# Performance work log

Hardware: AMD Instinct MI355X
Metric: run time of the kernel (lower is better)

## Reference

```python
import jax, jax.numpy as jnp
import numpy as np

B, D, K = 32, 64, 26      # batch, n_objects, per-object feature dim
QST = 256                  # question embedding size
G = [512, 512, 512, 512, 512, 512, 28]  # g_layers (last = n_answers)
IN = 2 * K                 # in_size = concat(x_i, x_j)
AGG = 4                    # aggregation + question injection position


def setup_inputs() -> dict:
    key = jax.random.key(0)
    ks = jax.random.split(key, 2 + 2 * len(G))
    inp = {
        "x": jax.random.normal(ks[0], (B, D, K), jnp.float32),
        "qst": jax.random.normal(ks[1], (B, QST), jnp.float32),
    }
    prev = IN
    for i, g in enumerate(G):
        d_in = prev + (QST if i == AGG else 0)
        inp[f"W{i}"] = jax.random.normal(ks[2 + 2 * i], (g, d_in), jnp.float32) * (1.0 / np.sqrt(d_in))
        inp[f"b{i}"] = jnp.zeros((g,), jnp.float32)
        prev = g
    return inp


def reference(x, qst, W0, b0, W1, b1, W2, b2, W3, b3, W4, b4, W5, b5, W6, b6):
    b, d, k = x.shape
    # all ordered pairs: x_full[b, p, q] = [x[b, q], x[b, p]]  (matches torch repeat/cat order)
    xi = jnp.broadcast_to(x[:, None, :, :], (b, d, d, k))
    xj = jnp.broadcast_to(x[:, :, None, :], (b, d, d, k))
    h = jnp.concatenate([xi, xj], axis=-1).reshape(b * d * d, 2 * k)
    Ws = [W0, W1, W2, W3, W4, W5, W6]
    bs = [b0, b1, b2, b3, b4, b5, b6]
    n = len(Ws)
    for i in range(n):
        if i == AGG:
            # sum-aggregation over all d^2 pairs, then question injection
            h = h.reshape(b, d * d, h.shape[-1]).sum(axis=1)  # [b, g]
            h = jnp.concatenate([h, qst], axis=1)             # [b, g+qst]
        h = h @ Ws[i].T + bs[i]
        if i != n - 1:
            h = jax.nn.relu(h)
    return jax.nn.log_softmax(h, axis=1)
```

## Files before the change

kernel.cpp:

```cpp
#include <hip/hip_runtime.h>
#include <math.h>


typedef __attribute__((ext_vector_type(8))) short bf16x8;
typedef __attribute__((ext_vector_type(4))) float f32x4;
typedef __attribute__((ext_vector_type(4))) unsigned int u32x4;

__device__ __forceinline__ unsigned short f2bf(float f) {
    union { float f; unsigned u; } x; x.f = f;
    unsigned r = x.u + 0x7fffu + ((x.u >> 16) & 1u);
    return (unsigned short)(r >> 16);
}

#define NPV_WP   98304
#define NPV_W0P  4096
#define NPV_W4   98304
#define NPV_W5   65536
#define NPV_TOTAL (NPV_WP + NPV_W0P + NPV_W4 + NPV_W5)
__global__ void k_prep(const float* __restrict__ W1, const float* __restrict__ W2,
                       const float* __restrict__ W3, const float* __restrict__ W0,
                       const float* __restrict__ W4, const float* __restrict__ W5,
                       unsigned short* __restrict__ Wp,
                       unsigned short* __restrict__ W0p,
                       float* __restrict__ W4v,
                       float* __restrict__ W5v)
{
    int f = blockIdx.x * 256 + threadIdx.x;
    if (f < NPV_WP) {
        int l = f >> 15, r = f & 32767;
        int n = r >> 6, kq = r & 63;
        const float* W = (l == 0) ? W1 : (l == 1) ? W2 : W3;
        const float* src = W + n * 512 + kq * 8;
        int s = kq >> 2, q4 = kq & 3;
        int wv = n >> 6, jj = (n >> 4) & 3, i16 = n & 15;
        int lane = q4 * 16 + i16;
        unsigned w[4];
        #pragma unroll
        for (int h = 0; h < 4; ++h)
            w[h] = (unsigned)f2bf(src[h * 2]) | ((unsigned)f2bf(src[h * 2 + 1]) << 16);
        *(u32x4*)(Wp + (size_t)l * 262144 + ((((wv * 16 + s) * 4 + jj) * 64 + lane) << 3))
            = (u32x4){w[0], w[1], w[2], w[3]};
    } else if (f < NPV_WP + NPV_W0P) {
        int g = f - NPV_WP;
        int n = g >> 3, kq = g & 7;
        int s = kq >> 2, q4 = kq & 3;
        int wv = n >> 6, jj = (n >> 4) & 3, i16 = n & 15;
        int lane = q4 * 16 + i16;
        unsigned w[4];
        #pragma unroll
        for (int h = 0; h < 4; ++h) {
            int k0 = kq * 8 + h * 2, k1 = k0 + 1;
            float f0 = (k0 < 52) ? W0[n * 52 + k0] : 0.f;
            float f1 = (k1 < 52) ? W0[n * 52 + k1] : 0.f;
            w[h] = (unsigned)f2bf(f0) | ((unsigned)f2bf(f1) << 16);
        }
        *(u32x4*)(W0p + ((((wv * 2 + s) * 4 + jj) * 64 + lane) << 3))
            = (u32x4){w[0], w[1], w[2], w[3]};
    } else if (f < NPV_WP + NPV_W0P + NPV_W4) {
        int g = f - (NPV_WP + NPV_W0P);
        int o = g / 192, kb = g % 192;
        float4 w = *(const float4*)(W4 + (size_t)o * 768 + kb * 4);
        *(float4*)(W4v + (size_t)kb * 2048 + o * 4) = w;
    } else {
        int g = f - (NPV_WP + NPV_W0P + NPV_W4);
        int o = g >> 7, kb = g & 127;
        float4 w = *(const float4*)(W5 + (size_t)o * 512 + kb * 4);
        *(float4*)(W5v + (size_t)kb * 2048 + o * 4) = w;
    }
}

__device__ __forceinline__ void store_h(const f32x4 (&acc)[4][4], const float* __restrict__ bl,
                                        unsigned short* hbuf, int wave, int i16, int q4, int lane)
{
    char* base = (char*)hbuf;
    #pragma unroll
    for (int j = 0; j < 4; ++j) {
        int col = (wave * 4 + j) * 16 + i16;
        int g = col >> 3;
        int e = g & 7;
        float bb = bl[col];
        char* colbase = base + g * 1024 + ((col & 7) << 1);
        #pragma unroll
        for (int mt = 0; mt < 4; ++mt) {
            #pragma unroll
            for (int r = 0; r < 4; ++r) {
                int row = mt * 16 + q4 * 4 + r;
                float v = fmaxf(acc[mt][j][r] + bb, 0.f);
                int vi = __float_as_int(v);
                int swi = __builtin_amdgcn_update_dpp(0, vi, 0xB1, 0xF, 0xF, true);
                if ((lane & 1) == 0) {
                    unsigned pk;
                    asm("v_cvt_pk_bf16_f32 %0, %1, %2" : "=v"(pk) : "v"(vi), "v"(swi));
                    int slot = row ^ e;
                    *(unsigned*)(colbase + slot * 16) = pk;
                }
            }
        }
    }
}

#define CLUSTER(AV0, AV1, AV2, AV3, BV, JJ)                                              \
    __builtin_amdgcn_s_setprio(1);                                                      \
    acc[0][JJ] = __builtin_amdgcn_mfma_f32_16x16x32_bf16(AV0, BV, acc[0][JJ], 0, 0, 0); \
    acc[1][JJ] = __builtin_amdgcn_mfma_f32_16x16x32_bf16(AV1, BV, acc[1][JJ], 0, 0, 0); \
    acc[2][JJ] = __builtin_amdgcn_mfma_f32_16x16x32_bf16(AV2, BV, acc[2][JJ], 0, 0, 0); \
    acc[3][JJ] = __builtin_amdgcn_mfma_f32_16x16x32_bf16(AV3, BV, acc[3][JJ], 0, 0, 0); \
    __builtin_amdgcn_s_setprio(0);                                                      \
    __builtin_amdgcn_sched_barrier(0);

__global__ __launch_bounds__(512, 2) void k_fused(
    const float* __restrict__ x,
    const unsigned short* __restrict__ Wp,
    const unsigned short* __restrict__ W0p,
    const float* __restrict__ b0, const float* __restrict__ b1,
    const float* __restrict__ b2, const float* __restrict__ b3,
    float* __restrict__ P)
{
    __shared__ __align__(16) unsigned short hsm[2 * 64 * 512];
    __shared__ __align__(16) unsigned short xs[8 * 64 * 8];
    int t = threadIdx.x;
    int blk = blockIdx.x;
    int b = blk >> 6, p = blk & 63;

    {
        int row = t >> 3, gr = t & 7;
        const float* xq = x + (size_t)(b * 64 + row) * 26;
        const float* xp = x + (size_t)(b * 64 + p) * 26;
        unsigned w[4];
        #pragma unroll
        for (int h = 0; h < 4; ++h) {
            int k0 = gr * 8 + h * 2;
            int k1 = k0 + 1;
            float f0 = (k0 < 26) ? xq[k0] : (k0 < 52 ? xp[k0 - 26] : 0.f);
            float f1 = (k1 < 26) ? xq[k1] : (k1 < 52 ? xp[k1 - 26] : 0.f);
            w[h] = (unsigned)f2bf(f0) | ((unsigned)f2bf(f1) << 16);
        }
        *(u32x4*)((char*)xs + gr * 1024 + ((row ^ gr) << 4)) = (u32x4){w[0], w[1], w[2], w[3]};
    }

    int wave = t >> 6, lane = t & 63;
    int i16 = lane & 15, q4 = lane >> 4;

    f32x4 acc[4][4];
    bf16x8 X0, X1, X2, X3, Y0, Y1, Y2, Y3;

    const unsigned short* Bb0base = Wp + wave * 32768 + lane * 8;

    __syncthreads();

    {
        #pragma unroll
        for (int mt = 0; mt < 4; ++mt)
            #pragma unroll
            for (int j = 0; j < 4; ++j)
                acc[mt][j] = (f32x4){0.f, 0.f, 0.f, 0.f};
        const unsigned short* Bw0 = W0p + wave * 4096 + lane * 8;
        const char* xb = (const char*)xs;
        #pragma unroll
        for (int s = 0; s < 2; ++s) {
            bf16x8 bfr[4];
            #pragma unroll
            for (int j = 0; j < 4; ++j)
                bfr[j] = *(const bf16x8*)(Bw0 + s * 2048 + j * 512);
            int g = s * 4 + q4;
            const char* A0 = xb + g * 1024 + ((i16 ^ g) << 4);
            #pragma unroll
            for (int mt = 0; mt < 4; ++mt) {
                bf16x8 a = *(const bf16x8*)(A0 + mt * 256);
                #pragma unroll
                for (int j = 0; j < 4; ++j)
                    acc[mt][j] = __builtin_amdgcn_mfma_f32_16x16x32_bf16(a, bfr[j], acc[mt][j], 0, 0, 0);
            }
        }
        X0 = *(const bf16x8*)(Bb0base);
        X1 = *(const bf16x8*)(Bb0base + 512);
        X2 = *(const bf16x8*)(Bb0base + 1024);
        X3 = *(const bf16x8*)(Bb0base + 1536);
        Y0 = *(const bf16x8*)(Bb0base + 2048);
        Y1 = *(const bf16x8*)(Bb0base + 2560);
        Y2 = *(const bf16x8*)(Bb0base + 3072);
        Y3 = *(const bf16x8*)(Bb0base + 3584);
        store_h(acc, b0, hsm, wave, i16, q4, lane);
    }
    __syncthreads();

    int A_even = (q4 << 10) + ((i16 ^ q4) << 4);
    int A_odd  = 4096 + (A_even ^ 64);

    #pragma unroll 1
    for (int l = 0; l < 3; ++l) {
        const float* bl = (l == 0) ? b1 : (l == 1) ? b2 : b3;
        const unsigned short* Bb = Bb0base + (size_t)l * 262144;
        const char* hb = (const char*)hsm + (l & 1) * 65536;
        const char* hbe = hb + A_even;
        const char* hbo = hb + A_odd;

        #pragma unroll
        for (int mt = 0; mt < 4; ++mt)
            #pragma unroll
            for (int j = 0; j < 4; ++j)
                acc[mt][j] = (f32x4){0.f, 0.f, 0.f, 0.f};

        bf16x8 aE0 = *(const bf16x8*)(hbe);
        bf16x8 aE1 = *(const bf16x8*)(hbe + 256);
        bf16x8 aE2 = *(const bf16x8*)(hbe + 512);
        bf16x8 aE3 = *(const bf16x8*)(hbe + 768);
        bf16x8 aO0, aO1, aO2, aO3;

        #pragma unroll 1
        for (int s = 0; s < 16; s += 2) {
            {
                const unsigned short* BX = Bb + ((s + 2 < 16) ? (s + 2) : 14) * 2048;
                const char* po = hbo + (s << 12);
                CLUSTER(aE0, aE1, aE2, aE3, X0, 0)
                X0 = *(const bf16x8*)(BX);
                aO0 = *(const bf16x8*)(po);
                aO1 = *(const bf16x8*)(po + 256);
                CLUSTER(aE0, aE1, aE2, aE3, X1, 1)
                X1 = *(const bf16x8*)(BX + 512);
                aO2 = *(const bf16x8*)(po + 512);
                aO3 = *(const bf16x8*)(po + 768);
                CLUSTER(aE0, aE1, aE2, aE3, X2, 2)
                X2 = *(const bf16x8*)(BX + 1024);
                CLUSTER(aE0, aE1, aE2, aE3, X3, 3)
                X3 = *(const bf16x8*)(BX + 1536);
            }
            {
                const unsigned short* BY = Bb + ((s + 3 < 16) ? (s + 3) : 15) * 2048;
                const char* pe = hbe + ((s + 2 < 16 ? s + 2 : 14) << 12);
                CLUSTER(aO0, aO1, aO2, aO3, Y0, 0)
                Y0 = *(const bf16x8*)(BY);
                aE0 = *(const bf16x8*)(pe);
                aE1 = *(const bf16x8*)(pe + 256);
                CLUSTER(aO0, aO1, aO2, aO3, Y1, 1)
                Y1 = *(const bf16x8*)(BY + 512);
                aE2 = *(const bf16x8*)(pe + 512);
                aE3 = *(const bf16x8*)(pe + 768);
                CLUSTER(aO0, aO1, aO2, aO3, Y2, 2)
                Y2 = *(const bf16x8*)(BY + 1024);
                CLUSTER(aO0, aO1, aO2, aO3, Y3, 3)
                Y3 = *(const bf16x8*)(BY + 1536);
            }
        }

        if (l < 2) {
            const unsigned short* Bn = Bb + 262144;
            X0 = *(const bf16x8*)(Bn);
            X1 = *(const bf16x8*)(Bn + 512);
            X2 = *(const bf16x8*)(Bn + 1024);
            X3 = *(const bf16x8*)(Bn + 1536);
            Y0 = *(const bf16x8*)(Bn + 2048);
            Y1 = *(const bf16x8*)(Bn + 2560);
            Y2 = *(const bf16x8*)(Bn + 3072);
            Y3 = *(const bf16x8*)(Bn + 3584);
            store_h(acc, bl, (unsigned short*)((char*)hsm + ((l + 1) & 1) * 65536),
                    wave, i16, q4, lane);
            __syncthreads();
        } else {
            #pragma unroll
            for (int j = 0; j < 4; ++j) {
                int col = (wave * 4 + j) * 16 + i16;
                float bb = bl[col];
                float sum = 0.f;
                #pragma unroll
                for (int mt = 0; mt < 4; ++mt)
                    #pragma unroll
                    for (int r = 0; r < 4; ++r)
                        sum += fmaxf(acc[mt][j][r] + bb, 0.f);
                sum += __shfl_xor(sum, 16);
                sum += __shfl_xor(sum, 32);
                if (q4 == 0) P[(size_t)blk * 512 + col] = sum;
            }
        }
    }
}

__global__ __launch_bounds__(64) void k_t1(const float* __restrict__ P,
                                           float* __restrict__ Z)
{
    int b = blockIdx.x >> 3, sl = blockIdx.x & 7;
    int col = sl * 64 + threadIdx.x;
    const float* Pb = P + (size_t)b * 64 * 512 + col;
    float s = 0.f;
    #pragma unroll 8
    for (int c = 0; c < 64; ++c) s += Pb[c * 512];
    Z[b * 512 + col] = s;
}

__global__ __launch_bounds__(256) void k_t2(
    const float* __restrict__ Z, const float* __restrict__ qst,
    const float* __restrict__ W4v, const float* __restrict__ b4,
    float* __restrict__ H4)
{
    int b = blockIdx.x >> 3, sl = blockIdx.x & 7;
    int t = threadIdx.x;
    __shared__ __align__(16) float z[768];
    __shared__ float ps[256];
    for (int i = t; i < 768; i += 256)
        z[i] = (i < 512) ? Z[b * 512 + i] : qst[b * 256 + (i - 512)];
    __syncthreads();
    int o = sl * 64 + (t & 63), hf = t >> 6;
    float acc = 0.f;
    const float4* Wv = (const float4*)W4v;
    const float4* z4 = (const float4*)z;
    #pragma unroll 4
    for (int kb = hf * 48; kb < hf * 48 + 48; ++kb) {
        float4 w = Wv[kb * 512 + o];
        float4 zz = z4[kb];
        acc = fmaf(w.x, zz.x, acc);
        acc = fmaf(w.y, zz.y, acc);
        acc = fmaf(w.z, zz.z, acc);
        acc = fmaf(w.w, zz.w, acc);
    }
    ps[t] = acc;
    __syncthreads();
    if (t < 64)
        H4[b * 512 + o] = fmaxf(ps[t] + ps[t + 64] + ps[t + 128] + ps[t + 192] + b4[o], 0.f);
}

__global__ __launch_bounds__(256) void k_t3(
    const float* __restrict__ H4,
    const float* __restrict__ W5v, const float* __restrict__ b5,
    float* __restrict__ H5)
{
    int b = blockIdx.x >> 3, sl = blockIdx.x & 7;
    int t = threadIdx.x;
    __shared__ __align__(16) float h4[512];
    __shared__ float ps[256];
    for (int i = t; i < 512; i += 256) h4[i] = H4[b * 512 + i];
    __syncthreads();
    int o = sl * 64 + (t & 63), hf = t >> 6;
    float acc = 0.f;
    const float4* Wv = (const float4*)W5v;
    const float4* h44 = (const float4*)h4;
    #pragma unroll 4
    for (int kb = hf * 32; kb < hf * 32 + 32; ++kb) {
        float4 w = Wv[kb * 512 + o];
        float4 hh = h44[kb];
        acc = fmaf(w.x, hh.x, acc);
        acc = fmaf(w.y, hh.y, acc);
        acc = fmaf(w.z, hh.z, acc);
        acc = fmaf(w.w, hh.w, acc);
    }
    ps[t] = acc;
    __syncthreads();
    if (t < 64)
        H5[b * 512 + o] = fmaxf(ps[t] + ps[t + 64] + ps[t + 128] + ps[t + 192] + b5[o], 0.f);
}

__global__ __launch_bounds__(512) void k_t4(
    const float* __restrict__ H5,
    const float* __restrict__ W6, const float* __restrict__ b6,
    float* __restrict__ out)
{
    int b = blockIdx.x, t = threadIdx.x;
    __shared__ __align__(16) float h5[512];
    __shared__ float logits[28];
    __shared__ float red[2];
    h5[t] = H5[b * 512 + t];
    __syncthreads();
    {
        int o = t >> 4, c = t & 15;
        if (o < 28) {
            float acc = 0.f;
            for (int k = c; k < 512; k += 16) acc = fmaf(W6[o * 512 + k], h5[k], acc);
            acc += __shfl_xor(acc, 1);
            acc += __shfl_xor(acc, 2);
            acc += __shfl_xor(acc, 4);
            acc += __shfl_xor(acc, 8);
            if (c == 0) logits[o] = acc + b6[o];
        }
    }
    __syncthreads();
    if (t == 0) {
        float mx = -1e30f;
        for (int cc = 0; cc < 28; ++cc) mx = fmaxf(mx, logits[cc]);
        float se = 0.f;
        for (int cc = 0; cc < 28; ++cc) se += expf(logits[cc] - mx);
        red[0] = mx; red[1] = logf(se);
    }
    __syncthreads();
    if (t < 28) out[b * 28 + t] = logits[t] - red[0] - red[1];
}

extern "C" void kernel_launch(void* const* d_in, const int* in_sizes, int n_in,
                              void* d_out, int out_size, void* d_ws, size_t ws_size,
                              hipStream_t stream)
{
    const float* x   = (const float*)d_in[0];
    const float* qst = (const float*)d_in[1];
    const float* W0  = (const float*)d_in[2];
    const float* b0  = (const float*)d_in[3];
    const float* W1  = (const float*)d_in[4];
    const float* b1  = (const float*)d_in[5];
    const float* W2  = (const float*)d_in[6];
    const float* b2  = (const float*)d_in[7];
    const float* W3  = (const float*)d_in[8];
    const float* b3  = (const float*)d_in[9];
    const float* W4  = (const float*)d_in[10];
    const float* b4  = (const float*)d_in[11];
    const float* W5  = (const float*)d_in[12];
    const float* b5  = (const float*)d_in[13];
    const float* W6  = (const float*)d_in[14];
    const float* b6  = (const float*)d_in[15];
    float* out = (float*)d_out;

    char* ws = (char*)d_ws;
    unsigned short* Wp  = (unsigned short*)(ws);
    unsigned short* W0p = (unsigned short*)(ws + 1572864);
    float*          W4v = (float*)(ws + 1638400);
    float*          W5v = (float*)(ws + 3211264);
    float*          P   = (float*)(ws + 4259840);
    float*          Z   = (float*)(ws + 8454144);
    float*          H4  = (float*)(ws + 8519680);
    float*          H5  = (float*)(ws + 8585216);

    k_prep <<<NPV_TOTAL / 256, 256, 0, stream>>>(W1, W2, W3, W0, W4, W5,
                                                 Wp, W0p, W4v, W5v);
    k_fused<<<2048, 512, 0, stream>>>(x, Wp, W0p, b0, b1, b2, b3, P);
    k_t1   <<<256, 64, 0, stream>>>(P, Z);
    k_t2   <<<256, 256, 0, stream>>>(Z, qst, W4v, b4, H4);
    k_t3   <<<256, 256, 0, stream>>>(H4, W5v, b5, H5);
    k_t4   <<<32, 512, 0, stream>>>(H5, W6, b6, out);
}
```

Baseline: 314.2 us.

## Stream weight tiles via global_load_lds double buffer and single-buffer activations

Replaces register-held weight B-fragment prefetch with direct global-to-LDS async loads (global_load_lds) into a per-wave double-buffered staging area, synchronized with vmcnt waits. To fit LDS, the ping-pong activation buffer is collapsed into a single buffer, adding an extra __syncthreads before each layer's store. The intent is to free VGPRs and hide weight-load latency. The cost is extra LDS reads per step, an added barrier per layer, and a manual vmcnt(4) wait whose correctness depends on the exact instruction ordering.

```diff
diff --git a/kernel.cpp b/kernel.cpp
--- a/kernel.cpp
+++ b/kernel.cpp
@@ -11,6 +11,15 @@
     unsigned r = x.u + 0x7fffu + ((x.u >> 16) & 1u);
     return (unsigned short)(r >> 16);
 }
+
+#define GLDS16(G, L)                                                        \
+    __builtin_amdgcn_global_load_lds(                                       \
+        (const __attribute__((address_space(1))) void*)(G),                 \
+        (__attribute__((address_space(3))) void*)(L), 16, 0, 0)
+
+#define WAIT_SLOT()                                        \
+    asm volatile("s_waitcnt vmcnt(4)" ::: "memory");       \
+    __builtin_amdgcn_sched_barrier(0);
 
 #define NPV_WP   98304
 #define NPV_W0P  4096
@@ -116,7 +125,8 @@
     const float* __restrict__ b2, const float* __restrict__ b3,
     float* __restrict__ P)
 {
-    __shared__ __align__(16) unsigned short hsm[2 * 64 * 512];
+    __shared__ __align__(16) unsigned short hsm[64 * 512];
+    __shared__ __align__(16) unsigned short Bst[2 * 8 * 2048];
     __shared__ __align__(16) unsigned short xs[8 * 64 * 8];
     int t = threadIdx.x;
     int blk = blockIdx.x;
@@ -142,9 +152,11 @@
     int i16 = lane & 15, q4 = lane >> 4;
 
     f32x4 acc[4][4];
-    bf16x8 X0, X1, X2, X3, Y0, Y1, Y2, Y3;
 
     const unsigned short* Bb0base = Wp + wave * 32768 + lane * 8;
+    unsigned short* Bw0 = Bst + wave * 2048;
+    unsigned short* Bw1 = Bw0 + 16384;
+    const char* Brd = (const char*)Bst + wave * 4096 + lane * 16;
 
     __syncthreads();
 
@@ -154,14 +166,14 @@
             #pragma unroll
             for (int j = 0; j < 4; ++j)
                 acc[mt][j] = (f32x4){0.f, 0.f, 0.f, 0.f};
-        const unsigned short* Bw0 = W0p + wave * 4096 + lane * 8;
+        const unsigned short* Bw = W0p + wave * 4096 + lane * 8;
         const char* xb = (const char*)xs;
         #pragma unroll
         for (int s = 0; s < 2; ++s) {
             bf16x8 bfr[4];
             #pragma unroll
             for (int j = 0; j < 4; ++j)
-                bfr[j] = *(const bf16x8*)(Bw0 + s * 2048 + j * 512);
+                bfr[j] = *(const bf16x8*)(Bw + s * 2048 + j * 512);
             int g = s * 4 + q4;
             const char* A0 = xb + g * 1024 + ((i16 ^ g) << 4);
             #pragma unroll
@@ -172,28 +184,22 @@
                     acc[mt][j] = __builtin_amdgcn_mfma_f32_16x16x32_bf16(a, bfr[j], acc[mt][j], 0, 0, 0);
             }
         }
-        X0 = *(const bf16x8*)(Bb0base);
-        X1 = *(const bf16x8*)(Bb0base + 512);
-        X2 = *(const bf16x8*)(Bb0base + 1024);
-        X3 = *(const bf16x8*)(Bb0base + 1536);
-        Y0 = *(const bf16x8*)(Bb0base + 2048);
-        Y1 = *(const bf16x8*)(Bb0base + 2560);
-        Y2 = *(const bf16x8*)(Bb0base + 3072);
-        Y3 = *(const bf16x8*)(Bb0base + 3584);
+        #pragma unroll
+        for (int j = 0; j < 4; ++j) GLDS16(Bb0base + j * 512,        Bw0 + j * 512);
+        #pragma unroll
+        for (int j = 0; j < 4; ++j) GLDS16(Bb0base + 2048 + j * 512, Bw1 + j * 512);
         store_h(acc, b0, hsm, wave, i16, q4, lane);
     }
     __syncthreads();
 
     int A_even = (q4 << 10) + ((i16 ^ q4) << 4);
-    int A_odd  = 4096 + (A_even ^ 64);
+    const char* hbe = (const char*)hsm + A_even;
+    const char* hbo = (const char*)hsm + 4096 + (A_even ^ 64);
 
     #pragma unroll 1
     for (int l = 0; l < 3; ++l) {
         const float* bl = (l == 0) ? b1 : (l == 1) ? b2 : b3;
         const unsigned short* Bb = Bb0base + (size_t)l * 262144;
-        const char* hb = (const char*)hsm + (l & 1) * 65536;
-        const char* hbe = hb + A_even;
-        const char* hbo = hb + A_odd;
 
         #pragma unroll
         for (int mt = 0; mt < 4; ++mt)
@@ -210,51 +216,58 @@
         #pragma unroll 1
         for (int s = 0; s < 16; s += 2) {
             {
-                const unsigned short* BX = Bb + ((s + 2 < 16) ? (s + 2) : 14) * 2048;
+                WAIT_SLOT()
+                bf16x8 b0v = *(const bf16x8*)(Brd);
+                bf16x8 b1v = *(const bf16x8*)(Brd + 1024);
+                bf16x8 b2v = *(const bf16x8*)(Brd + 2048);
+                bf16x8 b3v = *(const bf16x8*)(Brd + 3072);
                 const char* po = hbo + (s << 12);
-                CLUSTER(aE0, aE1, aE2, aE3, X0, 0)
-                X0 = *(const bf16x8*)(BX);
+                CLUSTER(aE0, aE1, aE2, aE3, b0v, 0)
                 aO0 = *(const bf16x8*)(po);
                 aO1 = *(const bf16x8*)(po + 256);
-                CLUSTER(aE0, aE1, aE2, aE3, X1, 1)
-                X1 = *(const bf16x8*)(BX + 512);
+                CLUSTER(aE0, aE1, aE2, aE3, b1v, 1)
                 aO2 = *(const bf16x8*)(po + 512);
                 aO3 = *(const bf16x8*)(po + 768);
-                CLUSTER(aE0, aE1, aE2, aE3, X2, 2)
-                X2 = *(const bf16x8*)(BX + 1024);
-                CLUSTER(aE0, aE1, aE2, aE3, X3, 3)
-                X3 = *(const bf16x8*)(BX + 1536);
+                CLUSTER(aE0, aE1, aE2, aE3, b2v, 2)
+                CLUSTER(aE0, aE1, aE2, aE3, b3v, 3)
+                int v = s + 2;
+                const unsigned short* gsrc = (v < 16) ? Bb + v * 2048
+                                           : (l < 2) ? Bb + 262144 + (v - 16) * 2048
+                                                     : Bb + (v - 2) * 2048;
+                GLDS16(gsrc,        Bw0);
+                GLDS16(gsrc + 512,  Bw0 + 512);
+                GLDS16(gsrc + 1024, Bw0 + 1024);
+                GLDS16(gsrc + 1536, Bw0 + 1536);
             }
             {
-                const unsigned short* BY = Bb + ((s + 3 < 16) ? (s + 3) : 15) * 2048;
+                WAIT_SLOT()
+                bf16x8 b0v = *(const bf16x8*)(Brd + 32768);
+                bf16x8 b1v = *(const bf16x8*)(Brd + 32768 + 1024);
+                bf16x8 b2v = *(const bf16x8*)(Brd + 32768 + 2048);
+                bf16x8 b3v = *(const bf16x8*)(Brd + 32768 + 3072);
                 const char* pe = hbe + ((s + 2 < 16 ? s + 2 : 14) << 12);
-                CLUSTER(aO0, aO1, aO2, aO3, Y0, 0)
-                Y0 = *(const bf16x8*)(BY);
+                CLUSTER(aO0, aO1, aO2, aO3, b0v, 0)
                 aE0 = *(const bf16x8*)(pe);
                 aE1 = *(const bf16x8*)(pe + 256);
-                CLUSTER(aO0, aO1, aO2, aO3, Y1, 1)
-                Y1 = *(const bf16x8*)(BY + 512);
+                CLUSTER(aO0, aO1, aO2, aO3, b1v, 1)
                 aE2 = *(const bf16x8*)(pe + 512);
                 aE3 = *(const bf16x8*)(pe + 768);
-                CLUSTER(aO0, aO1, aO2, aO3, Y2, 2)
-                Y2 = *(const bf16x8*)(BY + 1024);
-                CLUSTER(aO0, aO1, aO2, aO3, Y3, 3)
-                Y3 = *(const bf16x8*)(BY + 1536);
+                CLUSTER(aO0, aO1, aO2, aO3, b2v, 2)
+                CLUSTER(aO0, aO1, aO2, aO3, b3v, 3)
+                int v = s + 3;
+                const unsigned short* gsrc = (v < 16) ? Bb + v * 2048
+                                           : (l < 2) ? Bb + 262144 + (v - 16) * 2048
+                                                     : Bb + (v - 2) * 2048;
+                GLDS16(gsrc,        Bw1);
+                GLDS16(gsrc + 512,  Bw1 + 512);
+                GLDS16(gsrc + 1024, Bw1 + 1024);
+                GLDS16(gsrc + 1536, Bw1 + 1536);
             }
         }
 
         if (l < 2) {
-            const unsigned short* Bn = Bb + 262144;
-            X0 = *(const bf16x8*)(Bn);
-            X1 = *(const bf16x8*)(Bn + 512);
-            X2 = *(const bf16x8*)(Bn + 1024);
-            X3 = *(const bf16x8*)(Bn + 1536);
-            Y0 = *(const bf16x8*)(Bn + 2048);
-            Y1 = *(const bf16x8*)(Bn + 2560);
-            Y2 = *(const bf16x8*)(Bn + 3072);
-            Y3 = *(const bf16x8*)(Bn + 3584);
-            store_h(acc, bl, (unsigned short*)((char*)hsm + ((l + 1) & 1) * 65536),
-                    wave, i16, q4, lane);
+            __syncthreads();
+            store_h(acc, bl, hsm, wave, i16, q4, lane);
             __syncthreads();
         } else {
             #pragma unroll
```

Result: slower. 331.0 us (+5.3%).
